# Performance work log

Hardware: AMD Instinct MI355X
Metric: run time of the kernel (lower is better)

Reference implementation:

```python
import jax, jax.numpy as jnp
import numpy as np
import math

B, T, LM, LD, LP, D = 32, 40, 24, 32, 16, 256
VM, VD, VP = 4000, 6000, 2000
LTOT = LM + LD + LP + 1


def _sdpa(q, k, v, scale=None):
    # softmax(q k^T [*scale]) v, over the last two dims (works for rank-3 and rank-4)
    a = jnp.matmul(q, jnp.swapaxes(k, -1, -2))
    if scale is not None:
        a = a * scale
    a = jax.nn.softmax(a, axis=-1)
    return jnp.matmul(a, v)


def _pos_table():
    # HiTANet-style sinusoidal table with a zero pad row at index 0
    pos = np.arange(T, dtype=np.float32)[:, None]
    j = np.arange(D)[None, :]
    ang = pos / np.power(10000.0, 2.0 * (j // 2) / float(D))
    pe = np.where(j % 2 == 0, np.sin(ang), np.cos(ang)).astype(np.float32)
    return jnp.asarray(np.concatenate([np.zeros((1, D), np.float32), pe], axis=0))


def setup_inputs():
    key = jax.random.key(0)
    ks = jax.random.split(key, 24)
    u = lambda k, shape, b: jax.random.uniform(k, shape, jnp.float32, -b, b)
    inp = {
        "med_codes": jax.random.randint(ks[0], (B, T, LM), 0, VM),
        "diag_codes": jax.random.randint(ks[1], (B, T, LD), 0, VD),
        "proc_codes": jax.random.randint(ks[2], (B, T, LP), 0, VP),
        "med_mask_code": (jax.random.uniform(ks[3], (B, T, LM, 1)) < 0.8).astype(jnp.float32),
        "diag_mask_code": (jax.random.uniform(ks[4], (B, T, LD, 1)) < 0.8).astype(jnp.float32),
        "proc_mask_code": (jax.random.uniform(ks[5], (B, T, LP, 1)) < 0.8).astype(jnp.float32),
        "seq_time_step": jax.random.uniform(ks[6], (B, T), jnp.float32) * 2.0,
        "input_len": jax.random.randint(ks[7], (B,), 1, T + 1),
        "emb_med": jax.random.normal(ks[8], (VM, D), jnp.float32) * 0.02,
        "emb_diag": jax.random.normal(ks[9], (VD, D), jnp.float32) * 0.02,
        "emb_proc": jax.random.normal(ks[10], (VP, D), jnp.float32) * 0.02,
        "bias_med": u(ks[11], (D,), 1.0 / math.sqrt(VM)),
        "W_sel": u(ks[12], (64, 1), 1.0),
        "b_sel": u(ks[13], (64,), 1.0),
        "W_time": u(ks[14], (D, 64), 1.0 / math.sqrt(64.0)),
        "b_time": u(ks[15], (D,), 1.0 / math.sqrt(64.0)),
        "Wg_med": u(ks[16], (D, D), 1.0 / math.sqrt(float(D))),
        "bg_med": u(ks[17], (D,), 1.0 / math.sqrt(float(D))),
        "Wg_diag": u(ks[18], (D, D), 1.0 / math.sqrt(float(D))),
        "bg_diag": u(ks[19], (D,), 1.0 / math.sqrt(float(D))),
        "Wg_proc": u(ks[20], (D, D), 1.0 / math.sqrt(float(D))),
        "bg_proc": u(ks[21], (D,), 1.0 / math.sqrt(float(D))),
        "hidden_size": 256,
    }
    return inp


def reference(med_codes, diag_codes, proc_codes, med_mask_code, diag_mask_code,
              proc_mask_code, seq_time_step, input_len, emb_med, emb_diag, emb_proc,
              bias_med, W_sel, b_sel, W_time, b_time, Wg_med, bg_med, Wg_diag,
              bg_diag, Wg_proc, bg_proc, hidden_size):
    scale = 1.0 / math.sqrt(hidden_size + 1e-7)

    # time encoding: W2(1 - tanh((W1 t + b1)^2)) + b2  -> [B,T,1,D]
    t = seq_time_step[:, :, None]                       # [B,T,1]
    tf = 1.0 - jnp.tanh((t @ W_sel.T + b_sel) ** 2)     # [B,T,64]
    tf = tf @ W_time.T + b_time                         # [B,T,D]
    time_feature = tf[:, :, None, :]                    # [B,T,1,D]

    # positional encoding: positions 1..len, 0 (pad row) beyond len
    pe = _pos_table()
    ar = jnp.arange(T)[None, :]
    pos_idx = jnp.where(ar < input_len[:, None], ar + 1, 0)
    output_pos = pe[pos_idx]                            # [B,T,D]

    # masked embedding gathers [B,T,L,D]
    out_med = emb_med[med_codes] * med_mask_code
    out_diag = emb_diag[diag_codes] * diag_mask_code
    out_proc = emb_proc[proc_codes] * proc_mask_code

    # time-gated sigmoid modulation
    def gate(out, Wg, bg):
        g = _sdpa(time_feature, out, out, scale)        # [B,T,1,D]
        g = jax.nn.sigmoid(g @ Wg.T + bg)
        return g * out                                  # broadcast over L

    out_med = gate(out_med, Wg_med, bg_med)
    out_diag = gate(out_diag, Wg_diag, bg_diag)
    out_proc = gate(out_proc, Wg_proc, bg_proc)

    # per-modality self-attention over flattened T*L tokens
    def visit_att(out, L):
        x = out.reshape(B, T * L, D)
        x = _sdpa(x, x, x, scale)
        return x.reshape(B, T, L, D)

    out_med = visit_att(out_med, LM)
    out_diag = visit_att(out_diag, LD)
    out_proc = visit_att(out_proc, LP)

    # concat-fusion self-attention over all code types + time token [B,T,LTOT,D]
    merge = jnp.concatenate([out_med, out_diag, out_proc, time_feature], axis=2)
    merge = _sdpa(merge, merge, merge, scale)

    # med branch (predDiag=False, predProc=False): re-concat of the splits == merge
    out_med = merge[:, :, :LM]
    merge_aux = merge.reshape(B * T, LTOT, D)
    med_trans = out_med.reshape(B * T, LM, D)
    med_att = _sdpa(med_trans, merge_aux, merge_aux)    # no scale (default None)
    out = med_att.sum(axis=1).reshape(B, T, D) + bias_med + output_pos
    return out  # dropout is identity at eval
```

## Files before the change

kernel.cpp:

```cpp
#include <hip/hip_runtime.h>
#include <hip/hip_bf16.h>
#include <math.h>

typedef float f32x4 __attribute__((ext_vector_type(4)));
typedef short s16x8 __attribute__((ext_vector_type(8)));
typedef unsigned short us;

__device__ __forceinline__ float bf2f(us u){
  union { unsigned int i; float f; } v; v.i = ((unsigned int)u) << 16; return v.f;
}
__device__ __forceinline__ us f2bf(float f){
  union { float f; unsigned int i; } v; v.f = f;
  unsigned int r = v.i + 0x7FFFu + ((v.i >> 16) & 1u);
  return (us)(r >> 16);
}
__device__ __forceinline__ float dot4(f32x4 a, f32x4 b){
  return a.x*b.x + a.y*b.y + a.z*b.z + a.w*b.w;
}
__device__ __forceinline__ f32x4 mfma16(s16x8 a, s16x8 b, f32x4 c){
  return __builtin_amdgcn_mfma_f32_16x16x32_bf16(a, b, c, 0, 0, 0);
}
__device__ __forceinline__ void gld16(const us* src, us* dst){
  __builtin_amdgcn_global_load_lds(
      (const __attribute__((address_space(1))) unsigned int*)src,
      (__attribute__((address_space(3))) unsigned int*)dst, 16, 0, 0);
}

#define VM_WAIT8()  asm volatile("s_waitcnt vmcnt(8)" ::: "memory")
#define VM_WAIT0()  asm volatile("s_waitcnt vmcnt(0)" ::: "memory")
#define LGKM_WAIT0() asm volatile("s_waitcnt lgkmcnt(0)" ::: "memory")
#define PRO_WAIT()  asm volatile("s_waitcnt vmcnt(8) lgkmcnt(0)" ::: "memory")
#define BAR()       __builtin_amdgcn_s_barrier()

__global__ __launch_bounds__(256) void tf_kernel(
    const float* __restrict__ seq, const float* __restrict__ Wsel,
    const float* __restrict__ bsel, const float* __restrict__ Wtime,
    const float* __restrict__ btime, float* __restrict__ tf)
{
  const int bt = blockIdx.x, tid = threadIdx.x;
  __shared__ float w1[64];
  float s = seq[bt];
  if (tid < 64){ float h = s*Wsel[tid] + bsel[tid]; w1[tid] = 1.0f - tanhf(h*h); }
  __syncthreads();
  const float* wrow = Wtime + (size_t)tid*64;
  float acc = btime[tid];
  #pragma unroll 8
  for (int j = 0; j < 64; ++j) acc += w1[j]*wrow[j];
  tf[(size_t)bt*256 + tid] = acc;
}

struct GateLds {
  float E[32*260];
  float sc[64];
  float tfs[256];
  float gs[256];
};

template<int L, int N>
__device__ __forceinline__ void gate_body(GateLds& S,
    const int* __restrict__ codes, const float* __restrict__ mask,
    const float* __restrict__ emb, const float* __restrict__ tf,
    const float* __restrict__ Wg, const float* __restrict__ bg,
    us* __restrict__ Xg, us* __restrict__ XgT, float scale, int bt)
{
  const int b = bt/40, t = bt - (bt/40)*40;
  const int tid = threadIdx.x, lane = tid & 63, wid = tid >> 6;

  S.tfs[tid] = tf[(size_t)bt*256 + tid];
  #pragma unroll
  for (int l = 0; l < L; ++l){
    int code = codes[bt*L + l];
    float m = mask[bt*L + l];
    S.E[l*260 + tid] = emb[(size_t)code*256 + tid] * m;
  }
  __syncthreads();

  constexpr int RPW = (L + 3)/4;
  #pragma unroll
  for (int rr = 0; rr < RPW; ++rr){
    int l = wid*RPW + rr;
    if (l < L){
      f32x4 e4 = *(const f32x4*)&S.E[l*260 + lane*4];
      f32x4 t4 = *(const f32x4*)&S.tfs[lane*4];
      float p = dot4(e4, t4);
      #pragma unroll
      for (int m = 1; m < 64; m <<= 1) p += __shfl_xor(p, m, 64);
      if (lane == 0) S.sc[l] = p * scale;
    }
  }
  __syncthreads();
  if (wid == 0){
    float p = (lane < L) ? __expf(S.sc[lane]) : 0.f;
    float ss = p;
    #pragma unroll
    for (int m = 1; m < 64; m <<= 1) ss += __shfl_xor(ss, m, 64);
    if (lane < L) S.sc[lane] = p / ss;
  }
  __syncthreads();

  float g = 0.f;
  #pragma unroll
  for (int l = 0; l < L; ++l) g += S.sc[l]*S.E[l*260 + tid];
  S.gs[tid] = g;
  __syncthreads();

  const float* wrow = Wg + (size_t)tid*256;
  float a2 = bg[tid];
  #pragma unroll
  for (int e = 0; e < 256; e += 4){
    f32x4 w4 = *(const f32x4*)&wrow[e];
    f32x4 g4 = *(const f32x4*)&S.gs[e];
    a2 += dot4(w4, g4);
  }
  float g2 = 1.f/(1.f + __expf(-a2));

  us tbuf[L];
  #pragma unroll
  for (int l = 0; l < L; ++l){
    us h = f2bf(g2 * S.E[l*260 + tid]);
    Xg[((size_t)b*N + t*L + l)*256 + tid] = h;
    tbuf[l] = h;
  }
  size_t tb = ((size_t)b*256 + tid)*N + (size_t)t*L;
  #pragma unroll
  for (int l = 0; l < L; l += 8){
    uint4 v;
    v.x = (unsigned)tbuf[l+0] | ((unsigned)tbuf[l+1] << 16);
    v.y = (unsigned)tbuf[l+2] | ((unsigned)tbuf[l+3] << 16);
    v.z = (unsigned)tbuf[l+4] | ((unsigned)tbuf[l+5] << 16);
    v.w = (unsigned)tbuf[l+6] | ((unsigned)tbuf[l+7] << 16);
    *(uint4*)&XgT[tb + l] = v;
  }
}

template<int L, int N>
__global__ __launch_bounds__(256) void gate_kernel(
    const int* codes, const float* mask, const float* emb, const float* tf,
    const float* Wg, const float* bg, us* Xg, us* XgT, float scale)
{
  __shared__ GateLds S;
  gate_body<L,N>(S, codes, mask, emb, tf, Wg, bg, Xg, XgT, scale, blockIdx.x);
}

__global__ __launch_bounds__(256) void gate_fused(
    const int* mc, const int* dc, const int* pc,
    const float* mm, const float* dm, const float* pm,
    const float* em, const float* ed, const float* ep,
    const float* tf,
    const float* Wgm, const float* bgm, const float* Wgd, const float* bgd,
    const float* Wgp, const float* bgp,
    us* Xm, us* XTm, us* Xd, us* XTd, us* Xp, us* XTp, float scale)
{
  __shared__ GateLds S;
  int bid = blockIdx.x;
  if (bid < 1280)      gate_body<24,960 >(S, mc, mm, em, tf, Wgm, bgm, Xm, XTm, scale, bid);
  else if (bid < 2560) gate_body<32,1280>(S, dc, dm, ed, tf, Wgd, bgd, Xd, XTd, scale, bid-1280);
  else                 gate_body<16,640 >(S, pc, pm, ep, tf, Wgp, bgp, Xp, XTp, scale, bid-2560);
}

struct VisitLds {
  us buf[33792];
  us ps[4*32*40];
};

__device__ __forceinline__ void stage_tile(VisitLds& S, int cur,
    const us* __restrict__ Xb, const us* __restrict__ XTb, int k0, int N_, int tid)
{
  const int wid = tid >> 6;
  us* KS = S.buf + cur*8192;
  us* VS = S.buf + 16384 + cur*8704;
  #pragma unroll
  for (int i = 0; i < 4; ++i){
    int c = tid + i*256;
    int row = c >> 5, ch = c & 31;
    gld16(Xb + (size_t)(k0 + row)*256 + (((ch*16) ^ ((row & 7) << 4)) >> 1),
          KS + (i*256 + wid*64)*8);
    int d = c >> 2, kslot = c & 3;
    gld16(XTb + (size_t)d*N_ + k0 + kslot*8,
          VS + (i*256 + wid*64)*8);
  }
}

template<int N>
__device__ __forceinline__ void visit_body(VisitLds& S,
    const us* __restrict__ Xb, const us* __restrict__ XTb,
    us* __restrict__ Outb, float scale, int q0)
{
  const int tid = threadIdx.x, lane = tid & 63, wid = tid >> 6;
  const int lc = lane & 15, lg = lane >> 4;

  s16x8 qf[2][8];
  #pragma unroll
  for (int qg = 0; qg < 2; ++qg)
    #pragma unroll
    for (int kk = 0; kk < 8; ++kk){
      int gr = q0 + wid*32 + qg*16 + lc;
      gr = gr < N ? gr : N-1;
      qf[qg][kk] = *(const s16x8*)(Xb + (size_t)gr*256 + kk*32 + lg*8);
    }

  for (int i = tid; i < 512; i += 256){
    us v = (i < 32) ? (us)0x3F80 : (us)0;
    S.buf[16384 + 8192 + i] = v;
    S.buf[25088 + 8192 + i] = v;
  }

  stage_tile(S, 0, Xb, XTb, 0, N, tid);
  stage_tile(S, 1, Xb, XTb, 32, N, tid);
  PRO_WAIT();
  BAR();

  f32x4 o[2][16];
  #pragma unroll
  for (int qg = 0; qg < 2; ++qg)
    #pragma unroll
    for (int dcc = 0; dcc < 16; ++dcc) o[qg][dcc] = (f32x4){0.f,0.f,0.f,0.f};
  f32x4 ls[2] = {(f32x4){0.f,0.f,0.f,0.f}, (f32x4){0.f,0.f,0.f,0.f}};

  us* pw = S.ps + wid*32*40;
  const int nt = N/32;

  auto compute_tile = [&](int c){
    const us* KS = S.buf + c*8192;
    const us* VS = S.buf + 16384 + c*8704;

    f32x4 s[2][2];
    #pragma unroll
    for (int qg = 0; qg < 2; ++qg)
      #pragma unroll
      for (int kc = 0; kc < 2; ++kc) s[qg][kc] = (f32x4){0.f,0.f,0.f,0.f};

    __builtin_amdgcn_s_setprio(1);
    #pragma unroll
    for (int kk = 0; kk < 8; ++kk){
      #pragma unroll
      for (int kc = 0; kc < 2; ++kc){
        int row = kc*16 + lc;
        int off = kk*64 + lg*16;
        s16x8 kb = *(const s16x8*)((const char*)KS + row*512 + (off ^ ((row & 7) << 4)));
        s[0][kc] = mfma16(qf[0][kk], kb, s[0][kc]);
        s[1][kc] = mfma16(qf[1][kk], kb, s[1][kc]);
      }
    }
    __builtin_amdgcn_s_setprio(0);

    #pragma unroll
    for (int qg = 0; qg < 2; ++qg){
      #pragma unroll
      for (int r = 0; r < 4; ++r){
        float p0 = __expf(s[qg][0][r] * scale);
        float p1 = __expf(s[qg][1][r] * scale);
        int prow = qg*16 + lg*4 + r;
        pw[prow*40 + lc]      = f2bf(p0);
        pw[prow*40 + 16 + lc] = f2bf(p1);
      }
    }

    s16x8 pa[2];
    #pragma unroll
    for (int qg = 0; qg < 2; ++qg)
      pa[qg] = *(const s16x8*)(pw + (qg*16 + lc)*40 + lg*8);

    __builtin_amdgcn_s_setprio(1);
    #pragma unroll
    for (int dcc = 0; dcc < 16; ++dcc){
      s16x8 vf = *(const s16x8*)(VS + (dcc*16 + lc)*32 + lg*8);
      o[0][dcc] = mfma16(pa[0], vf, o[0][dcc]);
      o[1][dcc] = mfma16(pa[1], vf, o[1][dcc]);
    }
    {
      s16x8 vf1 = *(const s16x8*)(VS + (256 + lc)*32 + lg*8);
      ls[0] = mfma16(pa[0], vf1, ls[0]);
      ls[1] = mfma16(pa[1], vf1, ls[1]);
    }
    __builtin_amdgcn_s_setprio(0);
  };

  for (int t = 0; t < nt; ++t){
    compute_tile(t & 1);
    if (t == nt-1) break;
    LGKM_WAIT0();
    BAR();
    if (t + 2 < nt){
      stage_tile(S, t & 1, Xb, XTb, (t+2)*32, N, tid);
      VM_WAIT8();
    } else {
      VM_WAIT0();
    }
    BAR();
  }

  #pragma unroll
  for (int qg = 0; qg < 2; ++qg){
    #pragma unroll
    for (int r = 0; r < 4; ++r){
      float lv = __shfl(ls[qg][r], lane & 48, 64);
      float inv = 1.f / lv;
      int grow = q0 + wid*32 + qg*16 + lg*4 + r;
      if (grow < N){
        #pragma unroll
        for (int dcc = 0; dcc < 16; ++dcc){
          Outb[(size_t)grow*256 + dcc*16 + lc] = f2bf(o[qg][dcc][r] * inv);
        }
      }
    }
  }
}

template<int N>
__global__ __launch_bounds__(256, 2) void visit_kernel(
    const us* Xg, const us* XgT, us* Out, float scale)
{
  __shared__ VisitLds S;
  const int b = blockIdx.y;
  visit_body<N>(S, Xg + (size_t)b*N*256, XgT + (size_t)b*256*N,
                Out + (size_t)b*N*256, scale, blockIdx.x*128);
}

__global__ __launch_bounds__(256, 2) void visit_fused(
    const us* Xm, const us* XTm, us* Am,
    const us* Xd, const us* XTd, us* Ad,
    const us* Xp, const us* XTp, us* Ap, float scale)
{
  __shared__ VisitLds S;
  int p = blockIdx.x;
  int l = (p & 7)*92 + (p >> 3);
  if (l < 256){
    int b = l >> 3, q0 = (l & 7)*128;
    visit_body<960>(S, Xm + (size_t)b*960*256, XTm + (size_t)b*256*960,
                    Am + (size_t)b*960*256, scale, q0);
  } else if (l < 576){
    int r = l - 256, b = r/10, q0 = (r - (r/10)*10)*128;
    visit_body<1280>(S, Xd + (size_t)b*1280*256, XTd + (size_t)b*256*1280,
                     Ad + (size_t)b*1280*256, scale, q0);
  } else {
    int r = l - 576, b = r/5, q0 = (r - (r/5)*5)*128;
    visit_body<640>(S, Xp + (size_t)b*640*256, XTp + (size_t)b*256*640,
                    Ap + (size_t)b*640*256, scale, q0);
  }
}

__global__ __launch_bounds__(512, 2) void merge_kernel(
    const us* __restrict__ Amed, const us* __restrict__ Adiag,
    const us* __restrict__ Aproc, const float* __restrict__ tf,
    const float* __restrict__ bias, const int* __restrict__ ilen,
    float* __restrict__ out, float scale)
{
  __shared__ alignas(16) us Mb[80*256];
  __shared__ alignas(16) us SrB[80*96];
  __shared__ alignas(16) us Pb[80*96];
  __shared__ alignas(16) us W1B[32*96];
  __shared__ float wj[73];
  __shared__ float uk[73];
  float* S2f = (float*)SrB;

  const int bt = blockIdx.x, b = bt/40, t = bt - (bt/40)*40;
  const int tid = threadIdx.x, lane = tid & 63, wid = tid >> 6;
  const int lc = lane & 15, lg = lane >> 4;

  for (int c = tid; c < 72*32; c += 512){
    int row = c >> 5, ch = c & 31;
    const us* src;
    if (row < 24)      src = Amed  + ((size_t)b*960  + t*24 + row)*256      + ch*8;
    else if (row < 56) src = Adiag + ((size_t)b*1280 + t*32 + (row-24))*256 + ch*8;
    else               src = Aproc + ((size_t)b*640  + t*16 + (row-56))*256 + ch*8;
    uint4 v = *(const uint4*)src;
    *(uint4*)((char*)Mb + row*512 + ((ch*16) ^ ((row & 7) << 4))) = v;
  }
  if (tid < 256) Mb[72*256 + tid] = f2bf(tf[(size_t)bt*256 + tid]);
  for (int c = tid; c < 7*32; c += 512){
    int row = 73 + (c >> 5), ch = c & 31;
    *(uint4*)((char*)Mb + row*512 + ch*16) = (uint4){0,0,0,0};
  }
  __syncthreads();

  for (int tt = wid; tt < 25; tt += 8){
    int ti = tt/5, tj = tt - (tt/5)*5;
    f32x4 s = (f32x4){0.f,0.f,0.f,0.f};
    #pragma unroll
    for (int kk = 0; kk < 8; ++kk){
      int ra = ti*16 + lc, rb = tj*16 + lc;
      int off = kk*64 + lg*16;
      s16x8 a  = *(const s16x8*)((const char*)Mb + ra*512 + (off ^ ((ra & 7) << 4)));
      s16x8 bb = *(const s16x8*)((const char*)Mb + rb*512 + (off ^ ((rb & 7) << 4)));
      s = mfma16(a, bb, s);
    }
    #pragma unroll
    for (int r = 0; r < 4; ++r)
      SrB[(ti*16 + lg*4 + r)*96 + tj*16 + lc] = f2bf(s[r]);
  }
  __syncthreads();

  for (int c = tid; c < 80*16; c += 512){
    int r = c >> 4;
    SrB[r*96 + 80 + (c & 15)] = 0;
  }
  for (int r = wid; r < 73; r += 8){
    float e0 = __expf(scale * bf2f(SrB[r*96 + lane]));
    float e1 = (lane < 9) ? __expf(scale * bf2f(SrB[r*96 + 64 + lane])) : 0.f;
    float ss = e0 + e1;
    #pragma unroll
    for (int m = 1; m < 64; m <<= 1) ss += __shfl_xor(ss, m, 64);
    float inv = 1.f/ss;
    Pb[r*96 + lane] = f2bf(e0 * inv);
    if (lane < 32) Pb[r*96 + 64 + lane] = (lane < 9) ? f2bf(e1*inv) : (us)0;
  }
  for (int c = tid; c < 7*96; c += 512){
    Pb[73*96 + c] = 0;
  }
  __syncthreads();

  for (int tt = wid; tt < 10; tt += 8){
    int ri = tt/5, cj = tt - (tt/5)*5;
    f32x4 s = (f32x4){0.f,0.f,0.f,0.f};
    #pragma unroll
    for (int kk = 0; kk < 3; ++kk){
      s16x8 a  = *(const s16x8*)(Pb  + (ri*16 + lc)*96 + kk*32 + lg*8);
      s16x8 bb = *(const s16x8*)(SrB + (cj*16 + lc)*96 + kk*32 + lg*8);
      s = mfma16(a, bb, s);
    }
    #pragma unroll
    for (int r = 0; r < 4; ++r)
      W1B[(ri*16 + lg*4 + r)*96 + cj*16 + lc] = f2bf(s[r]);
  }
  if (tid < 512){
    W1B[(tid >> 4)*96 + 80 + (tid & 15)] = 0;
  }
  __syncthreads();

  for (int tt = wid; tt < 10; tt += 8){
    int ri = tt/5, cj = tt - (tt/5)*5;
    f32x4 s = (f32x4){0.f,0.f,0.f,0.f};
    #pragma unroll
    for (int kk = 0; kk < 3; ++kk){
      s16x8 a  = *(const s16x8*)(W1B + (ri*16 + lc)*96 + kk*32 + lg*8);
      s16x8 bb = *(const s16x8*)(Pb  + (cj*16 + lc)*96 + kk*32 + lg*8);
      s = mfma16(a, bb, s);
    }
    #pragma unroll
    for (int r = 0; r < 4; ++r)
      S2f[(ri*16 + lg*4 + r)*84 + cj*16 + lc] = s[r];
  }
  __syncthreads();

  for (int r = wid; r < 24; r += 8){
    float e0 = __expf(S2f[r*84 + lane]);
    float e1 = (lane < 9) ? __expf(S2f[r*84 + 64 + lane]) : 0.f;
    float ss = e0 + e1;
    #pragma unroll
    for (int m = 1; m < 64; m <<= 1) ss += __shfl_xor(ss, m, 64);
    float inv = 1.f/ss;
    S2f[r*84 + lane] = e0*inv;
    if (lane < 12) S2f[r*84 + 64 + lane] = (lane < 9) ? e1*inv : 0.f;
  }
  __syncthreads();

  if (tid < 73){
    float a = 0.f;
    #pragma unroll
    for (int i = 0; i < 24; ++i) a += S2f[i*84 + tid];
    wj[tid] = a;
  }
  __syncthreads();
  if (tid < 73){
    float a = 0.f;
    for (int j = 0; j < 73; ++j) a += wj[j] * bf2f(Pb[j*96 + tid]);
    uk[tid] = a;
  }
  __syncthreads();

  if (tid < 256){
    float acc = bias[tid];
    if (t < ilen[b]){
      float ex = (float)(2*(tid>>1)) * (1.0f/256.0f);
      float dv = powf(10000.f, ex);
      float ang = (float)t / dv;
      acc += (tid & 1) ? cosf(ang) : sinf(ang);
    }
    for (int k = 0; k < 73; ++k){
      us m = *(const us*)((const char*)Mb + k*512 + ((tid*2) ^ ((k & 7) << 4)));
      acc += uk[k] * bf2f(m);
    }
    out[(size_t)bt*256 + tid] = acc;
  }
}

extern "C" void kernel_launch(void* const* d_in, const int* in_sizes, int n_in,
                              void* d_out, int out_size, void* d_ws, size_t ws_size,
                              hipStream_t stream)
{
  (void)in_sizes; (void)n_in; (void)out_size;

  const int*   med_codes = (const int*)  d_in[0];
  const int*   diag_codes= (const int*)  d_in[1];
  const int*   proc_codes= (const int*)  d_in[2];
  const float* med_mask  = (const float*)d_in[3];
  const float* diag_mask = (const float*)d_in[4];
  const float* proc_mask = (const float*)d_in[5];
  const float* seq_time  = (const float*)d_in[6];
  const int*   input_len = (const int*)  d_in[7];
  const float* emb_med   = (const float*)d_in[8];
  const float* emb_diag  = (const float*)d_in[9];
  const float* emb_proc  = (const float*)d_in[10];
  const float* bias_med  = (const float*)d_in[11];
  const float* W_sel     = (const float*)d_in[12];
  const float* b_sel     = (const float*)d_in[13];
  const float* W_time    = (const float*)d_in[14];
  const float* b_time    = (const float*)d_in[15];
  const float* Wg_med    = (const float*)d_in[16];
  const float* bg_med    = (const float*)d_in[17];
  const float* Wg_diag   = (const float*)d_in[18];
  const float* bg_diag   = (const float*)d_in[19];
  const float* Wg_proc   = (const float*)d_in[20];
  const float* bg_proc   = (const float*)d_in[21];

  const float scale = (float)(1.0 / sqrt(256.0 + 1e-7));

  char* ws = (char*)d_ws;
  const size_t sz_tf = (size_t)1280*256*4;
  const size_t szA_m = (size_t)32*960*256*2;
  const size_t szA_d = (size_t)32*1280*256*2;
  const size_t szA_p = (size_t)32*640*256*2;

  size_t off = 0;
  float* tf   = (float*)(ws + off); off += sz_tf;
  us* Am      = (us*)(ws + off);    off += szA_m;
  us* Ad      = (us*)(ws + off);    off += szA_d;
  us* Ap      = (us*)(ws + off);    off += szA_p;

  const size_t fused_need = off + 2*(szA_m + szA_d + szA_p);
  tf_kernel<<<1280, 256, 0, stream>>>(seq_time, W_sel, b_sel, W_time, b_time, tf);

  if (ws_size >= fused_need){
    us* Xm  = (us*)(ws + off); off += szA_m;
    us* XTm = (us*)(ws + off); off += szA_m;
    us* Xd  = (us*)(ws + off); off += szA_d;
    us* XTd = (us*)(ws + off); off += szA_d;
    us* Xp  = (us*)(ws + off); off += szA_p;
    us* XTp = (us*)(ws + off); off += szA_p;

    gate_fused<<<3840, 256, 0, stream>>>(
        med_codes, diag_codes, proc_codes, med_mask, diag_mask, proc_mask,
        emb_med, emb_diag, emb_proc, tf,
        Wg_med, bg_med, Wg_diag, bg_diag, Wg_proc, bg_proc,
        Xm, XTm, Xd, XTd, Xp, XTp, scale);

    visit_fused<<<736, 256, 0, stream>>>(Xm, XTm, Am, Xd, XTd, Ad, Xp, XTp, Ap, scale);
  } else {
    us* Xg  = (us*)(ws + off);
    us* XgT = (us*)(ws + off + szA_d);

    gate_kernel<24,960><<<1280, 256, 0, stream>>>(med_codes, med_mask, emb_med, tf, Wg_med, bg_med, Xg, XgT, scale);
    visit_kernel<960><<<dim3(8,32), 256, 0, stream>>>(Xg, XgT, Am, scale);

    gate_kernel<32,1280><<<1280, 256, 0, stream>>>(diag_codes, diag_mask, emb_diag, tf, Wg_diag, bg_diag, Xg, XgT, scale);
    visit_kernel<1280><<<dim3(10,32), 256, 0, stream>>>(Xg, XgT, Ad, scale);

    gate_kernel<16,640><<<1280, 256, 0, stream>>>(proc_codes, proc_mask, emb_proc, tf, Wg_proc, bg_proc, Xg, XgT, scale);
    visit_kernel<640><<<dim3(5,32), 256, 0, stream>>>(Xg, XgT, Ap, scale);
  }

  merge_kernel<<<1280, 512, 0, stream>>>(Am, Ad, Ap, tf, bias_med, input_len, (float*)d_out, scale);
}
```

Before: 354.2 us.

## Single-buffer visit attention LDS with split K/V staging, alias merge LDS

```diff
diff --git a/kernel.cpp b/kernel.cpp
--- a/kernel.cpp
+++ b/kernel.cpp
@@ -26,11 +26,11 @@
       (__attribute__((address_space(3))) unsigned int*)dst, 16, 0, 0);
 }
 
-#define VM_WAIT8()  asm volatile("s_waitcnt vmcnt(8)" ::: "memory")
-#define VM_WAIT0()  asm volatile("s_waitcnt vmcnt(0)" ::: "memory")
+#define VM_WAIT4()   asm volatile("s_waitcnt vmcnt(4)" ::: "memory")
+#define WAIT_ALL()   asm volatile("s_waitcnt vmcnt(0) lgkmcnt(0)" ::: "memory")
 #define LGKM_WAIT0() asm volatile("s_waitcnt lgkmcnt(0)" ::: "memory")
-#define PRO_WAIT()  asm volatile("s_waitcnt vmcnt(8) lgkmcnt(0)" ::: "memory")
-#define BAR()       __builtin_amdgcn_s_barrier()
+#define BAR()        __builtin_amdgcn_s_barrier()
+#define SCHED_FENCE() __builtin_amdgcn_sched_barrier(0)
 
 __global__ __launch_bounds__(256) void tf_kernel(
     const float* __restrict__ seq, const float* __restrict__ Wsel,
@@ -159,25 +159,32 @@
 }
 
 struct VisitLds {
-  us buf[33792];
+  us ks[8192];
+  us vs[8704];
   us ps[4*32*40];
 };
 
-__device__ __forceinline__ void stage_tile(VisitLds& S, int cur,
-    const us* __restrict__ Xb, const us* __restrict__ XTb, int k0, int N_, int tid)
+__device__ __forceinline__ void stage_K(VisitLds& S, const us* __restrict__ Xb,
+                                        int k0, int tid)
 {
   const int wid = tid >> 6;
-  us* KS = S.buf + cur*8192;
-  us* VS = S.buf + 16384 + cur*8704;
   #pragma unroll
   for (int i = 0; i < 4; ++i){
     int c = tid + i*256;
     int row = c >> 5, ch = c & 31;
     gld16(Xb + (size_t)(k0 + row)*256 + (((ch*16) ^ ((row & 7) << 4)) >> 1),
-          KS + (i*256 + wid*64)*8);
+          S.ks + (i*256 + wid*64)*8);
+  }
+}
+__device__ __forceinline__ void stage_V(VisitLds& S, const us* __restrict__ XTb,
+                                        int k0, int N_, int tid)
+{
+  const int wid = tid >> 6;
+  #pragma unroll
+  for (int i = 0; i < 4; ++i){
+    int c = tid + i*256;
     int d = c >> 2, kslot = c & 3;
-    gld16(XTb + (size_t)d*N_ + k0 + kslot*8,
-          VS + (i*256 + wid*64)*8);
+    gld16(XTb + (size_t)d*N_ + k0 + kslot*8, S.vs + (i*256 + wid*64)*8);
   }
 }
 
@@ -199,15 +206,16 @@
       qf[qg][kk] = *(const s16x8*)(Xb + (size_t)gr*256 + kk*32 + lg*8);
     }
 
-  for (int i = tid; i < 512; i += 256){
-    us v = (i < 32) ? (us)0x3F80 : (us)0;
-    S.buf[16384 + 8192 + i] = v;
-    S.buf[25088 + 8192 + i] = v;
-  }
-
-  stage_tile(S, 0, Xb, XTb, 0, N, tid);
-  stage_tile(S, 1, Xb, XTb, 32, N, tid);
-  PRO_WAIT();
+  for (int i = tid; i < 512; i += 256)
+    S.vs[8192 + i] = (i < 32) ? (us)0x3F80 : (us)0;
+
+  SCHED_FENCE();
+  stage_K(S, Xb, 0, tid);
+  SCHED_FENCE();
+  stage_V(S, XTb, 0, N, tid);
+  SCHED_FENCE();
+  VM_WAIT4();
+  LGKM_WAIT0();
   BAR();
 
   f32x4 o[2][16];
@@ -220,10 +228,7 @@
   us* pw = S.ps + wid*32*40;
   const int nt = N/32;
 
-  auto compute_tile = [&](int c){
-    const us* KS = S.buf + c*8192;
-    const us* VS = S.buf + 16384 + c*8704;
-
+  for (int t = 0; t < nt; ++t){
     f32x4 s[2][2];
     #pragma unroll
     for (int qg = 0; qg < 2; ++qg)
@@ -237,7 +242,7 @@
       for (int kc = 0; kc < 2; ++kc){
         int row = kc*16 + lc;
         int off = kk*64 + lg*16;
-        s16x8 kb = *(const s16x8*)((const char*)KS + row*512 + (off ^ ((row & 7) << 4)));
+        s16x8 kb = *(const s16x8*)((const char*)S.ks + row*512 + (off ^ ((row & 7) << 4)));
         s[0][kc] = mfma16(qf[0][kk], kb, s[0][kc]);
         s[1][kc] = mfma16(qf[1][kk], kb, s[1][kc]);
       }
@@ -255,39 +260,38 @@
         pw[prow*40 + 16 + lc] = f2bf(p1);
       }
     }
-
     s16x8 pa[2];
     #pragma unroll
     for (int qg = 0; qg < 2; ++qg)
       pa[qg] = *(const s16x8*)(pw + (qg*16 + lc)*40 + lg*8);
 
+    WAIT_ALL();
+    BAR();
+    if (t + 1 < nt) stage_K(S, Xb, (t+1)*32, tid);
+
     __builtin_amdgcn_s_setprio(1);
     #pragma unroll
     for (int dcc = 0; dcc < 16; ++dcc){
-      s16x8 vf = *(const s16x8*)(VS + (dcc*16 + lc)*32 + lg*8);
+      s16x8 vf = *(const s16x8*)(S.vs + (dcc*16 + lc)*32 + lg*8);
       o[0][dcc] = mfma16(pa[0], vf, o[0][dcc]);
       o[1][dcc] = mfma16(pa[1], vf, o[1][dcc]);
     }
     {
-      s16x8 vf1 = *(const s16x8*)(VS + (256 + lc)*32 + lg*8);
+      s16x8 vf1 = *(const s16x8*)(S.vs + (256 + lc)*32 + lg*8);
       ls[0] = mfma16(pa[0], vf1, ls[0]);
       ls[1] = mfma16(pa[1], vf1, ls[1]);
     }
     __builtin_amdgcn_s_setprio(0);
-  };
-
-  for (int t = 0; t < nt; ++t){
-    compute_tile(t & 1);
-    if (t == nt-1) break;
-    LGKM_WAIT0();
-    BAR();
-    if (t + 2 < nt){
-      stage_tile(S, t & 1, Xb, XTb, (t+2)*32, N, tid);
-      VM_WAIT8();
-    } else {
-      VM_WAIT0();
-    }
-    BAR();
+
+    if (t + 1 < nt){
+      LGKM_WAIT0();
+      BAR();
+      SCHED_FENCE();
+      stage_V(S, XTb, (t+1)*32, N, tid);
+      SCHED_FENCE();
+      VM_WAIT4();
+      BAR();
+    }
   }
 
   #pragma unroll
@@ -308,7 +312,7 @@
 }
 
 template<int N>
-__global__ __launch_bounds__(256, 2) void visit_kernel(
+__global__ __launch_bounds__(256, 3) void visit_kernel(
     const us* Xg, const us* XgT, us* Out, float scale)
 {
   __shared__ VisitLds S;
@@ -317,7 +321,7 @@
                 Out + (size_t)b*N*256, scale, blockIdx.x*128);
 }
 
-__global__ __launch_bounds__(256, 2) void visit_fused(
+__global__ __launch_bounds__(256, 3) void visit_fused(
     const us* Xm, const us* XTm, us* Am,
     const us* Xd, const us* XTd, us* Ad,
     const us* Xp, const us* XTp, us* Ap, float scale)
@@ -325,14 +329,14 @@
   __shared__ VisitLds S;
   int p = blockIdx.x;
   int l = (p & 7)*92 + (p >> 3);
-  if (l < 256){
-    int b = l >> 3, q0 = (l & 7)*128;
+  if (l < 320){
+    int b = l/10, q0 = (l - (l/10)*10)*128;
+    visit_body<1280>(S, Xd + (size_t)b*1280*256, XTd + (size_t)b*256*1280,
+                     Ad + (size_t)b*1280*256, scale, q0);
+  } else if (l < 576){
+    int r = l - 320, b = r >> 3, q0 = (r & 7)*128;
     visit_body<960>(S, Xm + (size_t)b*960*256, XTm + (size_t)b*256*960,
                     Am + (size_t)b*960*256, scale, q0);
-  } else if (l < 576){
-    int r = l - 256, b = r/10, q0 = (r - (r/10)*10)*128;
-    visit_body<1280>(S, Xd + (size_t)b*1280*256, XTd + (size_t)b*256*1280,
-                     Ad + (size_t)b*1280*256, scale, q0);
   } else {
     int r = l - 576, b = r/5, q0 = (r - (r/5)*5)*128;
     visit_body<640>(S, Xp + (size_t)b*640*256, XTp + (size_t)b*256*640,
@@ -340,18 +344,19 @@
   }
 }
 
-__global__ __launch_bounds__(512, 2) void merge_kernel(
+__global__ __launch_bounds__(512, 4) void merge_kernel(
     const us* __restrict__ Amed, const us* __restrict__ Adiag,
     const us* __restrict__ Aproc, const float* __restrict__ tf,
     const float* __restrict__ bias, const int* __restrict__ ilen,
     float* __restrict__ out, float scale)
 {
-  __shared__ alignas(16) us Mb[80*256];
+  __shared__ alignas(16) us A[80*256];
   __shared__ alignas(16) us SrB[80*96];
-  __shared__ alignas(16) us Pb[80*96];
-  __shared__ alignas(16) us W1B[32*96];
-  __shared__ float wj[73];
-  __shared__ float uk[73];
+  us* Mb  = A;
+  us* Pb  = A;
+  us* W1B = A + 7680;
+  float* wj  = (float*)(A + 10752);
+  float* uk  = (float*)(A + 10912);
   float* S2f = (float*)SrB;
 
   const int bt = blockIdx.x, b = bt/40, t = bt - (bt/40)*40;
@@ -477,10 +482,16 @@
       float ang = (float)t / dv;
       acc += (tid & 1) ? cosf(ang) : sinf(ang);
     }
-    for (int k = 0; k < 73; ++k){
-      us m = *(const us*)((const char*)Mb + k*512 + ((tid*2) ^ ((k & 7) << 4)));
-      acc += uk[k] * bf2f(m);
-    }
+    const us* Am_ = Amed  + ((size_t)b*960  + t*24)*256 + tid;
+    #pragma unroll 4
+    for (int k = 0; k < 24; ++k) acc += uk[k]      * bf2f(Am_[k*256]);
+    const us* Ad_ = Adiag + ((size_t)b*1280 + t*32)*256 + tid;
+    #pragma unroll 4
+    for (int k = 0; k < 32; ++k) acc += uk[24 + k] * bf2f(Ad_[k*256]);
+    const us* Ap_ = Aproc + ((size_t)b*640  + t*16)*256 + tid;
+    #pragma unroll 4
+    for (int k = 0; k < 16; ++k) acc += uk[56 + k] * bf2f(Ap_[k*256]);
+    acc += uk[72] * tf[(size_t)bt*256 + tid];
     out[(size_t)bt*256 + tid] = acc;
   }
 }
```

Result: slower. 725.2 us (+104.7%).

## Use constant ones operand for row sums, alias merge LDS, reorder visit blocks

Applied to the files above, without the earlier changes.

```diff
diff --git a/kernel.cpp b/kernel.cpp
--- a/kernel.cpp
+++ b/kernel.cpp
@@ -26,11 +26,11 @@
       (__attribute__((address_space(3))) unsigned int*)dst, 16, 0, 0);
 }
 
-#define VM_WAIT8()  asm volatile("s_waitcnt vmcnt(8)" ::: "memory")
-#define VM_WAIT0()  asm volatile("s_waitcnt vmcnt(0)" ::: "memory")
+#define VM_WAIT8()   asm volatile("s_waitcnt vmcnt(8)" ::: "memory")
+#define VM_WAIT0()   asm volatile("s_waitcnt vmcnt(0)" ::: "memory")
 #define LGKM_WAIT0() asm volatile("s_waitcnt lgkmcnt(0)" ::: "memory")
-#define PRO_WAIT()  asm volatile("s_waitcnt vmcnt(8) lgkmcnt(0)" ::: "memory")
-#define BAR()       __builtin_amdgcn_s_barrier()
+#define PRO_WAIT()   asm volatile("s_waitcnt vmcnt(8) lgkmcnt(0)" ::: "memory")
+#define BAR()        __builtin_amdgcn_s_barrier()
 
 __global__ __launch_bounds__(256) void tf_kernel(
     const float* __restrict__ seq, const float* __restrict__ Wsel,
@@ -172,12 +172,12 @@
   #pragma unroll
   for (int i = 0; i < 4; ++i){
     int c = tid + i*256;
-    int row = c >> 5, ch = c & 31;
-    gld16(Xb + (size_t)(k0 + row)*256 + (((ch*16) ^ ((row & 7) << 4)) >> 1),
-          KS + (i*256 + wid*64)*8);
+    int row = c >> 5, off = (c & 31) * 16;
+    gld16(Xb + (size_t)(k0 + row)*256 + ((off ^ ((row & 7) << 4)) >> 1),
+          KS + (size_t)(wid*64 + i*256)*8);
     int d = c >> 2, kslot = c & 3;
     gld16(XTb + (size_t)d*N_ + k0 + kslot*8,
-          VS + (i*256 + wid*64)*8);
+          VS + (size_t)(wid*64 + i*256)*8);
   }
 }
 
@@ -199,11 +199,9 @@
       qf[qg][kk] = *(const s16x8*)(Xb + (size_t)gr*256 + kk*32 + lg*8);
     }
 
-  for (int i = tid; i < 512; i += 256){
-    us v = (i < 32) ? (us)0x3F80 : (us)0;
-    S.buf[16384 + 8192 + i] = v;
-    S.buf[25088 + 8192 + i] = v;
-  }
+  s16x8 ONES;
+  #pragma unroll
+  for (int i = 0; i < 8; ++i) ONES[i] = (short)0x3F80;
 
   stage_tile(S, 0, Xb, XTb, 0, N, tid);
   stage_tile(S, 1, Xb, XTb, 32, N, tid);
@@ -268,11 +266,8 @@
       o[0][dcc] = mfma16(pa[0], vf, o[0][dcc]);
       o[1][dcc] = mfma16(pa[1], vf, o[1][dcc]);
     }
-    {
-      s16x8 vf1 = *(const s16x8*)(VS + (256 + lc)*32 + lg*8);
-      ls[0] = mfma16(pa[0], vf1, ls[0]);
-      ls[1] = mfma16(pa[1], vf1, ls[1]);
-    }
+    ls[0] = mfma16(pa[0], ONES, ls[0]);
+    ls[1] = mfma16(pa[1], ONES, ls[1]);
     __builtin_amdgcn_s_setprio(0);
   };
 
@@ -294,8 +289,7 @@
   for (int qg = 0; qg < 2; ++qg){
     #pragma unroll
     for (int r = 0; r < 4; ++r){
-      float lv = __shfl(ls[qg][r], lane & 48, 64);
-      float inv = 1.f / lv;
+      float inv = 1.f / ls[qg][r];
       int grow = q0 + wid*32 + qg*16 + lg*4 + r;
       if (grow < N){
         #pragma unroll
@@ -325,14 +319,14 @@
   __shared__ VisitLds S;
   int p = blockIdx.x;
   int l = (p & 7)*92 + (p >> 3);
-  if (l < 256){
-    int b = l >> 3, q0 = (l & 7)*128;
+  if (l < 320){
+    int b = l/10, q0 = (l - (l/10)*10)*128;
+    visit_body<1280>(S, Xd + (size_t)b*1280*256, XTd + (size_t)b*256*1280,
+                     Ad + (size_t)b*1280*256, scale, q0);
+  } else if (l < 576){
+    int r = l - 320, b = r >> 3, q0 = (r & 7)*128;
     visit_body<960>(S, Xm + (size_t)b*960*256, XTm + (size_t)b*256*960,
                     Am + (size_t)b*960*256, scale, q0);
-  } else if (l < 576){
-    int r = l - 256, b = r/10, q0 = (r - (r/10)*10)*128;
-    visit_body<1280>(S, Xd + (size_t)b*1280*256, XTd + (size_t)b*256*1280,
-                     Ad + (size_t)b*1280*256, scale, q0);
   } else {
     int r = l - 576, b = r/5, q0 = (r - (r/5)*5)*128;
     visit_body<640>(S, Xp + (size_t)b*640*256, XTp + (size_t)b*256*640,
@@ -340,18 +334,19 @@
   }
 }
 
-__global__ __launch_bounds__(512, 2) void merge_kernel(
+__global__ __launch_bounds__(512, 4) void merge_kernel(
     const us* __restrict__ Amed, const us* __restrict__ Adiag,
     const us* __restrict__ Aproc, const float* __restrict__ tf,
     const float* __restrict__ bias, const int* __restrict__ ilen,
     float* __restrict__ out, float scale)
 {
-  __shared__ alignas(16) us Mb[80*256];
+  __shared__ alignas(16) us A[80*256];
   __shared__ alignas(16) us SrB[80*96];
-  __shared__ alignas(16) us Pb[80*96];
-  __shared__ alignas(16) us W1B[32*96];
-  __shared__ float wj[73];
-  __shared__ float uk[73];
+  us* Mb  = A;
+  us* Pb  = A;
+  us* W1B = A + 7680;
+  float* wj  = (float*)(A + 10752);
+  float* uk  = (float*)(A + 10912);
   float* S2f = (float*)SrB;
 
   const int bt = blockIdx.x, b = bt/40, t = bt - (bt/40)*40;
@@ -477,10 +472,16 @@
       float ang = (float)t / dv;
       acc += (tid & 1) ? cosf(ang) : sinf(ang);
     }
-    for (int k = 0; k < 73; ++k){
-      us m = *(const us*)((const char*)Mb + k*512 + ((tid*2) ^ ((k & 7) << 4)));
-      acc += uk[k] * bf2f(m);
-    }
+    const us* Am_ = Amed  + ((size_t)b*960  + t*24)*256 + tid;
+    #pragma unroll 4
+    for (int k = 0; k < 24; ++k) acc += uk[k]      * bf2f(Am_[k*256]);
+    const us* Ad_ = Adiag + ((size_t)b*1280 + t*32)*256 + tid;
+    #pragma unroll 4
+    for (int k = 0; k < 32; ++k) acc += uk[24 + k] * bf2f(Ad_[k*256]);
+    const us* Ap_ = Aproc + ((size_t)b*640  + t*16)*256 + tid;
+    #pragma unroll 4
+    for (int k = 0; k < 16; ++k) acc += uk[56 + k] * bf2f(Ap_[k*256]);
+    acc += uk[72] * tf[(size_t)bt*256 + tid];
     out[(size_t)bt*256 + tid] = acc;
   }
 }
```

After: 355.6 us. Within noise of the previous version (+0.4%).
